# Kernel optimization log

Measured on AMD Instinct MI355X. Metric: run time of the kernel, lower is better.

## Reference

```python
import jax, jax.numpy as jnp
import numpy as np

NUM_DOCS = 1024  # fill_max of doc_indices

def setup_inputs() -> dict:
    key = jax.random.key(0)
    k1, k2, k3 = jax.random.split(key, 3)
    N, D, E = 262144, 1024, 64
    x = jax.random.normal(k1, (N, D), dtype=jnp.float32)
    doc_indices = jax.random.randint(k2, (N,), 0, NUM_DOCS, dtype=jnp.int64)
    W_gate = jax.random.normal(k3, (E, D), dtype=jnp.float32)
    return {"x": x, "doc_indices": doc_indices, "W_gate": W_gate}

def reference(x, doc_indices, W_gate):
    # gate linear + softmax: [N, E]
    logits = jnp.einsum('nd,ed->ne', x, W_gate)
    w = jax.nn.softmax(logits, axis=-1)

    seg = doc_indices.astype(jnp.int32)
    E = w.shape[-1]
    # one-pass segment reductions replacing the per-document Python loop
    sum_w = jax.ops.segment_sum(w, seg, num_segments=NUM_DOCS)          # [D, E]
    sum_w2 = jax.ops.segment_sum(w * w, seg, num_segments=NUM_DOCS)     # [D, E]
    counts = jax.ops.segment_sum(jnp.ones_like(w[:, :1]), seg, num_segments=NUM_DOCS)  # [D, 1]
    safe_n = jnp.maximum(counts, 1.0)
    centroid = sum_w / safe_n                                            # [D, E]
    # per-doc sum of squared deviations: sum(w^2) - n * centroid^2
    ssd = jnp.sum(sum_w2 - safe_n * centroid * centroid, axis=-1)        # [D]
    n = counts[:, 0]
    per_doc_mse = ssd / (safe_n[:, 0] * E)                               # mean over n_d*E elements
    valid = n > 1.0                                                      # docs with >1 token contribute
    penalty_sum = jnp.sum(jnp.where(valid, per_doc_mse, 0.0))
    num_unique = jnp.sum((n > 0.0).astype(jnp.float32))
    doc_penalty = penalty_sum / num_unique
    return (w, doc_penalty)
```

## Files before the change

### kernel.cpp

```cpp
#include <hip/hip_runtime.h>
#include <math.h>

#define NROWS 262144
#define DDIM  1024
#define EEXP  64
#define NDOCS 1024
#define BM    128
#define HB    64
#define RPB   (NROWS / HB)
#define NGEMM (NROWS / BM)

typedef __attribute__((ext_vector_type(8)))  __bf16 bf16x8;
typedef __attribute__((ext_vector_type(16))) float  f32x16;
typedef unsigned short ushort_t;
typedef unsigned int   uint_t;


__global__ __launch_bounds__(256) void conv_hist_kernel(const float* __restrict__ Wg,
                                                        ushort_t* __restrict__ Wf,
                                                        const int* __restrict__ idx,
                                                        int* __restrict__ hist_slices) {
    if (blockIdx.x < 512) {
        const int i = blockIdx.x * 256 + threadIdx.x;
        const int j = i & 7;
        const int l = (i >> 3) & 63;
        const int f = (i >> 9) & 7;
        const int T = i >> 12;
        const int cl = l & 31;
        const int hi = l >> 5;
        const int e  = cl + 32 * ((f >> 1) & 1);
        const int k  = T * 32 + 16 * (f & 1) + 8 * hi + j;
        const float wv = Wg[e * DDIM + k];
        const uint_t b = __float_as_uint(wv);
        ushort_t out;
        if (f < 4) {
            out = (ushort_t)(b >> 16);
        } else {
            const float lov = wv - __uint_as_float(b & 0xFFFF0000u);
            out = (ushort_t)(__float_as_uint(lov) >> 16);
        }
        Wf[i] = out;
    } else {
        __shared__ int lh[NDOCS];
        const int bh = blockIdx.x - 512;
        const int t  = threadIdx.x;
        for (int i = t; i < NDOCS; i += 256) lh[i] = 0;
        __syncthreads();
        const int base = bh * RPB;
        for (int i = t; i < RPB; i += 256) atomicAdd(&lh[idx[base + i]], 1);
        __syncthreads();
        for (int i = t; i < NDOCS; i += 256) hist_slices[bh * NDOCS + i] = lh[i];
    }
}

__global__ __launch_bounds__(1024) void scan_kernel(const int* __restrict__ hist_slices,
                                                    int* __restrict__ offsets,
                                                    int* __restrict__ cursor,
                                                    float* __restrict__ pen_sum,
                                                    float* __restrict__ uniq,
                                                    int* __restrict__ done_count) {
    __shared__ int sbuf[NDOCS];
    const int t = threadIdx.x;
    int my = 0;
    #pragma unroll 4
    for (int b = 0; b < HB; ++b) my += hist_slices[b * NDOCS + t];
    sbuf[t] = my;
    __syncthreads();
    for (int off = 1; off < NDOCS; off <<= 1) {
        int add = (t >= off) ? sbuf[t - off] : 0;
        __syncthreads();
        sbuf[t] += add;
        __syncthreads();
    }
    const int excl = sbuf[t] - my;
    offsets[t] = excl;
    cursor[t]  = excl;
    if (t == NDOCS - 1) offsets[NDOCS] = sbuf[t];
    if (t == 0) { pen_sum[0] = 0.0f; uniq[0] = 0.0f; done_count[0] = 0; }
}

__device__ __forceinline__ void gl2lds16(const float* g, float* l) {
    __builtin_amdgcn_global_load_lds(
        (const __attribute__((address_space(1))) void*)g,
        (__attribute__((address_space(3))) void*)l,
        16, 0, 0);
}

#define VMCNT(N)  asm volatile("s_waitcnt vmcnt(" #N ")" ::: "memory")

struct WT { bf16x8 h00, h01, h10, h11, m00, m01, m10, m11; };

__global__ __launch_bounds__(256, 2) void gemm_scatter_kernel(
    const float*    __restrict__ x,
    const ushort_t* __restrict__ Wf,
    const int*      __restrict__ idx,
    int*            __restrict__ cursor,
    int*            __restrict__ sorted_rows,
    float*          __restrict__ w_out)
{
    __shared__ float xs[2][8192];

    if (blockIdx.x >= NGEMM) {
        int* lh    = (int*)&xs[0][0];
        int* lbase = lh + NDOCS;
        int* lc    = lbase + NDOCS;
        const int bh = blockIdx.x - NGEMM;
        const int t  = threadIdx.x;
        for (int i = t; i < NDOCS; i += 256) { lh[i] = 0; lc[i] = 0; }
        __syncthreads();
        const int base = bh * RPB;
        for (int i = t; i < RPB; i += 256) atomicAdd(&lh[idx[base + i]], 1);
        __syncthreads();
        for (int i = t; i < NDOCS; i += 256) {
            const int c = lh[i];
            if (c) lbase[i] = atomicAdd(&cursor[i], c);
        }
        __syncthreads();
        for (int i = t; i < RPB; i += 256) {
            const int r = base + i;
            const int d = idx[r];
            const int p = atomicAdd(&lc[d], 1);
            sorted_rows[lbase[d] + p] = r;
        }
        return;
    }

    const int t   = threadIdx.x;
    const int w   = t >> 6;
    const int l   = t & 63;
    const int cl  = l & 31;
    const int hi  = l >> 5;
    const size_t br = (size_t)blockIdx.x * BM;

    f32x16 acc0 = {};
    f32x16 acc1 = {};
    WT wA, wB;

    union u8b { uint_t u[4]; bf16x8 v; };

#define LOAD_WF(DST, T2) do {                                                          \
        const ushort_t* p_ = Wf + ((size_t)(T2) * 8 * 64 + l) * 8;                     \
        DST.h00 = *(const bf16x8*)(p_ + 0 * 512);                                      \
        DST.h01 = *(const bf16x8*)(p_ + 1 * 512);                                      \
        DST.h10 = *(const bf16x8*)(p_ + 2 * 512);                                      \
        DST.h11 = *(const bf16x8*)(p_ + 3 * 512);                                      \
        DST.m00 = *(const bf16x8*)(p_ + 4 * 512);                                      \
        DST.m01 = *(const bf16x8*)(p_ + 5 * 512);                                      \
        DST.m10 = *(const bf16x8*)(p_ + 6 * 512);                                      \
        DST.m11 = *(const bf16x8*)(p_ + 7 * 512);                                      \
    } while (0)

#define STAGE_X2(BUF, SUP) do {                                                        \
        float* xb_ = &xs[BUF][w * 2048];                                               \
        _Pragma("unroll")                                                              \
        for (int i_ = 0; i_ < 8; ++i_) {                                               \
            const int row_ = i_ * 4 + (l >> 4);                                        \
            const int u_   = (l & 15) ^ (row_ & 15);                                   \
            const float* gp_ = x + (br + w * 32 + row_) * DDIM + (SUP) * 64 + u_ * 4;  \
            gl2lds16(gp_, xb_ + i_ * 256);                                             \
        } } while (0)

#define SPLIT8(A, B, AH, AL) do {                                                      \
        const float av_[8] = {A.x, A.y, A.z, A.w, B.x, B.y, B.z, B.w};                 \
        _Pragma("unroll")                                                              \
        for (int p_ = 0; p_ < 4; ++p_) {                                               \
            const uint_t b0_ = __float_as_uint(av_[2 * p_]);                           \
            const uint_t b1_ = __float_as_uint(av_[2 * p_ + 1]);                       \
            AH.u[p_] = (b0_ >> 16) | (b1_ & 0xFFFF0000u);                              \
            const float l0_ = av_[2 * p_]     - __uint_as_float(b0_ & 0xFFFF0000u);    \
            const float l1_ = av_[2 * p_ + 1] - __uint_as_float(b1_ & 0xFFFF0000u);    \
            AL.u[p_] = (__float_as_uint(l0_) >> 16) | (__float_as_uint(l1_) & 0xFFFF0000u); \
        } } while (0)

#define COMPUTE(BUF, TT, WV) do {                                                      \
        const float* xb_ = &xs[BUF][w * 2048];                                         \
        const int blk_ = (cl >> 2) * 256 + (cl & 3) * 64;                              \
        const int ku_  = (TT) * 8 + hi * 2;                                            \
        const int sw_  = cl & 15;                                                      \
        const float4 a0_ = *(const float4*)&xb_[blk_ + (((ku_ + 0) ^ sw_) * 4)];       \
        const float4 a1_ = *(const float4*)&xb_[blk_ + (((ku_ + 1) ^ sw_) * 4)];       \
        const float4 a2_ = *(const float4*)&xb_[blk_ + (((ku_ + 4) ^ sw_) * 4)];       \
        const float4 a3_ = *(const float4*)&xb_[blk_ + (((ku_ + 5) ^ sw_) * 4)];       \
        u8b ah0, al0, ah1, al1;                                                        \
        SPLIT8(a0_, a1_, ah0, al0);                                                    \
        SPLIT8(a2_, a3_, ah1, al1);                                                    \
        acc0 = __builtin_amdgcn_mfma_f32_32x32x16_bf16(ah0.v, WV.h00, acc0, 0, 0, 0);  \
        acc1 = __builtin_amdgcn_mfma_f32_32x32x16_bf16(ah0.v, WV.h10, acc1, 0, 0, 0);  \
        acc0 = __builtin_amdgcn_mfma_f32_32x32x16_bf16(ah0.v, WV.m00, acc0, 0, 0, 0);  \
        acc1 = __builtin_amdgcn_mfma_f32_32x32x16_bf16(ah0.v, WV.m10, acc1, 0, 0, 0);  \
        acc0 = __builtin_amdgcn_mfma_f32_32x32x16_bf16(al0.v, WV.h00, acc0, 0, 0, 0);  \
        acc1 = __builtin_amdgcn_mfma_f32_32x32x16_bf16(al0.v, WV.h10, acc1, 0, 0, 0);  \
        acc0 = __builtin_amdgcn_mfma_f32_32x32x16_bf16(ah1.v, WV.h01, acc0, 0, 0, 0);  \
        acc1 = __builtin_amdgcn_mfma_f32_32x32x16_bf16(ah1.v, WV.h11, acc1, 0, 0, 0);  \
        acc0 = __builtin_amdgcn_mfma_f32_32x32x16_bf16(ah1.v, WV.m01, acc0, 0, 0, 0);  \
        acc1 = __builtin_amdgcn_mfma_f32_32x32x16_bf16(ah1.v, WV.m11, acc1, 0, 0, 0);  \
        acc0 = __builtin_amdgcn_mfma_f32_32x32x16_bf16(al1.v, WV.h01, acc0, 0, 0, 0);  \
        acc1 = __builtin_amdgcn_mfma_f32_32x32x16_bf16(al1.v, WV.h11, acc1, 0, 0, 0);  \
    } while (0)

    LOAD_WF(wA, 0);
    STAGE_X2(0, 0);
    LOAD_WF(wB, 1);
    STAGE_X2(1, 1);
    VMCNT(16);
    COMPUTE(0, 0, wA);
    LOAD_WF(wA, 2);
    VMCNT(16);
    COMPUTE(0, 1, wB);

    #pragma unroll 1
    for (int S = 1; S < 15; ++S) {
        const int cb = S & 1;
        LOAD_WF(wB, 2 * S + 1);
        STAGE_X2(cb ^ 1, S + 1);
        VMCNT(16);
        COMPUTE(cb, 0, wA);
        LOAD_WF(wA, 2 * S + 2);
        VMCNT(16);
        COMPUTE(cb, 1, wB);
    }
    LOAD_WF(wB, 31);
    VMCNT(8);
    COMPUTE(1, 0, wA);
    VMCNT(0);
    COMPUTE(1, 1, wB);

    const size_t orow_base = br + (size_t)w * 32;
    #pragma unroll
    for (int r = 0; r < 16; ++r) {
        const int row = (r & 3) + 8 * (r >> 2) + 4 * hi;
        const float v0 = acc0[r];
        const float v1 = acc1[r];
        float m = fmaxf(v0, v1);
        m = fmaxf(m, __shfl_xor(m, 1));
        m = fmaxf(m, __shfl_xor(m, 2));
        m = fmaxf(m, __shfl_xor(m, 4));
        m = fmaxf(m, __shfl_xor(m, 8));
        m = fmaxf(m, __shfl_xor(m, 16));
        const float e0 = __expf(v0 - m);
        const float e1 = __expf(v1 - m);
        float s = e0 + e1;
        s += __shfl_xor(s, 1);
        s += __shfl_xor(s, 2);
        s += __shfl_xor(s, 4);
        s += __shfl_xor(s, 8);
        s += __shfl_xor(s, 16);
        const float inv = 1.0f / s;
        float* wo = w_out + (orow_base + row) * EEXP;
        wo[cl]      = e0 * inv;
        wo[32 + cl] = e1 * inv;
    }
#undef LOAD_WF
#undef STAGE_X2
#undef SPLIT8
#undef COMPUTE
}

__global__ __launch_bounds__(256) void segsum_final_kernel(
    const float* __restrict__ w,
    const int*   __restrict__ sorted_rows,
    const int*   __restrict__ offsets,
    float*       __restrict__ pen_sum,
    float*       __restrict__ uniq,
    int*         __restrict__ done_count,
    float*       __restrict__ pen_out)
{
    __shared__ int rows_s[512];
    __shared__ float ls1[4][64], ls2[4][64];

    const int d  = blockIdx.x;
    const int t  = threadIdx.x;
    const int e  = t & 63;
    const int rg = t >> 6;
    const int start = offsets[d];
    const int end   = offsets[d + 1];
    const int n     = end - start;

    for (int i = t; i < n && i < 512; i += 256) rows_s[i] = sorted_rows[start + i];
    __syncthreads();

    float s1 = 0.0f, s2 = 0.0f;
    for (int i = rg; i < n; i += 4) {
        const int row = (i < 512) ? rows_s[i] : sorted_rows[start + i];
        const float v = w[(size_t)row * EEXP + e];
        s1 += v;
        s2 += v * v;
    }

    ls1[rg][e] = s1;
    ls2[rg][e] = s2;
    __syncthreads();

    if (t < 64) {
        const float a = ls1[0][e] + ls1[1][e] + ls1[2][e] + ls1[3][e];
        const float b = ls2[0][e] + ls2[1][e] + ls2[2][e] + ls2[3][e];
        const float safe = fmaxf((float)n, 1.0f);
        float contrib = b - a * a / safe;
        #pragma unroll
        for (int off = 32; off > 0; off >>= 1)
            contrib += __shfl_down(contrib, off);
        if (e == 0) {
            if (n > 1) atomicAdd(pen_sum, contrib / (safe * (float)EEXP));
            if (n > 0) atomicAdd(uniq, 1.0f);
        }
    }
    __syncthreads();
    if (t == 0) {
        __threadfence();
        const int prev = atomicAdd(done_count, 1);
        if (prev == NDOCS - 1) {
            __threadfence();
            pen_out[0] = pen_sum[0] / uniq[0];
        }
    }
}

extern "C" void kernel_launch(void* const* d_in, const int* in_sizes, int n_in,
                              void* d_out, int out_size, void* d_ws, size_t ws_size,
                              hipStream_t stream) {
    const float* x   = (const float*)d_in[0];
    const int*   idx = (const int*)d_in[1];
    const float* Wg  = (const float*)d_in[2];

    float* out   = (float*)d_out;
    float* w_out = out;
    float* pen   = out + (size_t)NROWS * EEXP;

    ushort_t* Wf     = (ushort_t*)d_ws;
    int* hist_slices = (int*)(Wf + 131072);
    int* sorted_rows = hist_slices + HB * NDOCS;
    int* offsets     = sorted_rows + NROWS;
    int* cursor      = offsets + NDOCS + 1;
    float* pen_sum   = (float*)(cursor + NDOCS);
    float* uniq      = pen_sum + 1;
    int* done_count  = (int*)(uniq + 1);

    conv_hist_kernel<<<512 + HB, 256, 0, stream>>>(Wg, Wf, idx, hist_slices);
    scan_kernel<<<1, 1024, 0, stream>>>(hist_slices, offsets, cursor, pen_sum, uniq, done_count);
    gemm_scatter_kernel<<<NGEMM + HB, 256, 0, stream>>>(x, Wf, idx, cursor, sorted_rows, w_out);
    segsum_final_kernel<<<NDOCS, 256, 0, stream>>>(w_out, sorted_rows, offsets, pen_sum, uniq, done_count, pen);
}
```

Baseline: 360.5 us.

## Restructure gate GEMM into 16-row tiles with K-split across waves

Replaces the 128-row-per-block 32x32 MFMA GEMM with 16x16x32 MFMA tiles where each block covers 8 row-tiles of 16 rows. The four waves split the 64 experts and the K dimension is walked in 256-wide chunks with a per-block rotated start to spread Wf/x access. Softmax now goes through an LDS transpose buffer, and occupancy rises to 4 blocks per CU with a smaller LDS footprint. The histogram/scatter blocks move to the front of the grid. The intent is better latency hiding and more resident waves, at the cost of more barriers and reloading W for every 16-row tile.

```diff
diff --git a/kernel.cpp b/kernel.cpp
--- a/kernel.cpp
+++ b/kernel.cpp
@@ -5,13 +5,14 @@
 #define DDIM  1024
 #define EEXP  64
 #define NDOCS 1024
-#define BM    128
 #define HB    64
 #define RPB   (NROWS / HB)
-#define NGEMM (NROWS / BM)
-
-typedef __attribute__((ext_vector_type(8)))  __bf16 bf16x8;
-typedef __attribute__((ext_vector_type(16))) float  f32x16;
+#define BMT   16
+#define TPB   8
+#define NGEMM (NROWS / (BMT * TPB))
+
+typedef __attribute__((ext_vector_type(8))) __bf16 bf16x8;
+typedef __attribute__((ext_vector_type(4))) float  f32x4;
 typedef unsigned short ushort_t;
 typedef unsigned int   uint_t;
 
@@ -21,19 +22,18 @@
                                                         const int* __restrict__ idx,
                                                         int* __restrict__ hist_slices) {
     if (blockIdx.x < 512) {
-        const int i = blockIdx.x * 256 + threadIdx.x;
-        const int j = i & 7;
-        const int l = (i >> 3) & 63;
-        const int f = (i >> 9) & 7;
-        const int T = i >> 12;
-        const int cl = l & 31;
-        const int hi = l >> 5;
-        const int e  = cl + 32 * ((f >> 1) & 1);
-        const int k  = T * 32 + 16 * (f & 1) + 8 * hi + j;
+        const int i  = blockIdx.x * 256 + threadIdx.x;
+        const int j  = i & 7;
+        const int l  = (i >> 3) & 63;
+        const int hl = (i >> 9) & 1;
+        const int eb = (i >> 10) & 3;
+        const int Tg = i >> 12;
+        const int e  = eb * 16 + (l & 15);
+        const int k  = Tg * 32 + (l >> 4) * 8 + j;
         const float wv = Wg[e * DDIM + k];
         const uint_t b = __float_as_uint(wv);
         ushort_t out;
-        if (f < 4) {
+        if (hl == 0) {
             out = (ushort_t)(b >> 16);
         } else {
             const float lov = wv - __uint_as_float(b & 0xFFFF0000u);
@@ -87,10 +87,10 @@
 }
 
 #define VMCNT(N)  asm volatile("s_waitcnt vmcnt(" #N ")" ::: "memory")
-
-struct WT { bf16x8 h00, h01, h10, h11, m00, m01, m10, m11; };
-
-__global__ __launch_bounds__(256, 2) void gemm_scatter_kernel(
+#define LGKM0()   asm volatile("s_waitcnt lgkmcnt(0)" ::: "memory")
+#define BAR()     do { __builtin_amdgcn_s_barrier(); asm volatile("" ::: "memory"); } while (0)
+
+__global__ __launch_bounds__(256, 4) void gemm_scatter_kernel(
     const float*    __restrict__ x,
     const ushort_t* __restrict__ Wf,
     const int*      __restrict__ idx,
@@ -98,13 +98,14 @@
     int*            __restrict__ sorted_rows,
     float*          __restrict__ w_out)
 {
-    __shared__ float xs[2][8192];
-
-    if (blockIdx.x >= NGEMM) {
+    __shared__ float xs[2][BMT * 256];
+    __shared__ float lsm[BMT * 68];
+
+    if (blockIdx.x < HB) {
         int* lh    = (int*)&xs[0][0];
         int* lbase = lh + NDOCS;
         int* lc    = lbase + NDOCS;
-        const int bh = blockIdx.x - NGEMM;
+        const int bh = blockIdx.x;
         const int t  = threadIdx.x;
         for (int i = t; i < NDOCS; i += 256) { lh[i] = 0; lc[i] = 0; }
         __syncthreads();
@@ -125,39 +126,42 @@
         return;
     }
 
-    const int t   = threadIdx.x;
-    const int w   = t >> 6;
-    const int l   = t & 63;
-    const int cl  = l & 31;
-    const int hi  = l >> 5;
-    const size_t br = (size_t)blockIdx.x * BM;
-
-    f32x16 acc0 = {};
-    f32x16 acc1 = {};
-    WT wA, wB;
+    const int gb   = blockIdx.x - HB;
+    const int t    = threadIdx.x;
+    const int w    = t >> 6;
+    const int l    = t & 63;
+    const int al16 = l & 15;
+    const int g2   = l >> 4;
+    const size_t br = (size_t)gb * (BMT * TPB);
+    const int s0   = gb & 3;
+
+    f32x4 acc = {0.f, 0.f, 0.f, 0.f};
+    bf16x8 wh0, wl0, wh1, wl1, wh2, wl2, wh3, wl3, wh4, wl4, wh5, wl5, wh6, wl6, wh7, wl7;
 
     union u8b { uint_t u[4]; bf16x8 v; };
 
-#define LOAD_WF(DST, T2) do {                                                          \
-        const ushort_t* p_ = Wf + ((size_t)(T2) * 8 * 64 + l) * 8;                     \
-        DST.h00 = *(const bf16x8*)(p_ + 0 * 512);                                      \
-        DST.h01 = *(const bf16x8*)(p_ + 1 * 512);                                      \
-        DST.h10 = *(const bf16x8*)(p_ + 2 * 512);                                      \
-        DST.h11 = *(const bf16x8*)(p_ + 3 * 512);                                      \
-        DST.m00 = *(const bf16x8*)(p_ + 4 * 512);                                      \
-        DST.m01 = *(const bf16x8*)(p_ + 5 * 512);                                      \
-        DST.m10 = *(const bf16x8*)(p_ + 6 * 512);                                      \
-        DST.m11 = *(const bf16x8*)(p_ + 7 * 512);                                      \
+#define LWT(T2, WH, WL) do {                                                           \
+        const ushort_t* p_ = Wf + ((size_t)((T2) * 8 + w * 2) * 64 + l) * 8;           \
+        WH = *(const bf16x8*)p_;                                                       \
+        WL = *(const bf16x8*)(p_ + 512);                                               \
     } while (0)
 
-#define STAGE_X2(BUF, SUP) do {                                                        \
-        float* xb_ = &xs[BUF][w * 2048];                                               \
+#define LOAD_W_ALL(S) do {                                                             \
+        LWT((S)*8 + 0, wh0, wl0); LWT((S)*8 + 1, wh1, wl1);                            \
+        LWT((S)*8 + 2, wh2, wl2); LWT((S)*8 + 3, wh3, wl3);                            \
+        LWT((S)*8 + 4, wh4, wl4); LWT((S)*8 + 5, wh5, wl5);                            \
+        LWT((S)*8 + 6, wh6, wl6); LWT((S)*8 + 7, wh7, wl7);                            \
+    } while (0)
+
+#define STAGE(BUF, P) do {                                                             \
+        const int rb_ = ((P) >> 2) * BMT;                                              \
+        const int kb_ = ((s0 + ((P) & 3)) & 3) * 256;                                  \
+        float* xb_ = &xs[BUF][0];                                                      \
         _Pragma("unroll")                                                              \
-        for (int i_ = 0; i_ < 8; ++i_) {                                               \
-            const int row_ = i_ * 4 + (l >> 4);                                        \
-            const int u_   = (l & 15) ^ (row_ & 15);                                   \
-            const float* gp_ = x + (br + w * 32 + row_) * DDIM + (SUP) * 64 + u_ * 4;  \
-            gl2lds16(gp_, xb_ + i_ * 256);                                             \
+        for (int i_ = 0; i_ < 4; ++i_) {                                               \
+            const int rl_ = w * 4 + i_;                                                \
+            const float* gp_ = x + (br + rb_ + rl_) * (size_t)DDIM + kb_ + ((l ^ rl_) * 4); \
+            gl2lds16(gp_, xb_ + rl_ * 256);                                            \
         } } while (0)
 
 #define SPLIT8(A, B, AH, AL) do {                                                      \
@@ -172,88 +176,93 @@
             AL.u[p_] = (__float_as_uint(l0_) >> 16) | (__float_as_uint(l1_) & 0xFFFF0000u); \
         } } while (0)
 
-#define COMPUTE(BUF, TT, WV) do {                                                      \
-        const float* xb_ = &xs[BUF][w * 2048];                                         \
-        const int blk_ = (cl >> 2) * 256 + (cl & 3) * 64;                              \
-        const int ku_  = (TT) * 8 + hi * 2;                                            \
-        const int sw_  = cl & 15;                                                      \
-        const float4 a0_ = *(const float4*)&xb_[blk_ + (((ku_ + 0) ^ sw_) * 4)];       \
-        const float4 a1_ = *(const float4*)&xb_[blk_ + (((ku_ + 1) ^ sw_) * 4)];       \
-        const float4 a2_ = *(const float4*)&xb_[blk_ + (((ku_ + 4) ^ sw_) * 4)];       \
-        const float4 a3_ = *(const float4*)&xb_[blk_ + (((ku_ + 5) ^ sw_) * 4)];       \
-        u8b ah0, al0, ah1, al1;                                                        \
-        SPLIT8(a0_, a1_, ah0, al0);                                                    \
-        SPLIT8(a2_, a3_, ah1, al1);                                                    \
-        acc0 = __builtin_amdgcn_mfma_f32_32x32x16_bf16(ah0.v, WV.h00, acc0, 0, 0, 0);  \
-        acc1 = __builtin_amdgcn_mfma_f32_32x32x16_bf16(ah0.v, WV.h10, acc1, 0, 0, 0);  \
-        acc0 = __builtin_amdgcn_mfma_f32_32x32x16_bf16(ah0.v, WV.m00, acc0, 0, 0, 0);  \
-        acc1 = __builtin_amdgcn_mfma_f32_32x32x16_bf16(ah0.v, WV.m10, acc1, 0, 0, 0);  \
-        acc0 = __builtin_amdgcn_mfma_f32_32x32x16_bf16(al0.v, WV.h00, acc0, 0, 0, 0);  \
-        acc1 = __builtin_amdgcn_mfma_f32_32x32x16_bf16(al0.v, WV.h10, acc1, 0, 0, 0);  \
-        acc0 = __builtin_amdgcn_mfma_f32_32x32x16_bf16(ah1.v, WV.h01, acc0, 0, 0, 0);  \
-        acc1 = __builtin_amdgcn_mfma_f32_32x32x16_bf16(ah1.v, WV.h11, acc1, 0, 0, 0);  \
-        acc0 = __builtin_amdgcn_mfma_f32_32x32x16_bf16(ah1.v, WV.m01, acc0, 0, 0, 0);  \
-        acc1 = __builtin_amdgcn_mfma_f32_32x32x16_bf16(ah1.v, WV.m11, acc1, 0, 0, 0);  \
-        acc0 = __builtin_amdgcn_mfma_f32_32x32x16_bf16(al1.v, WV.h01, acc0, 0, 0, 0);  \
-        acc1 = __builtin_amdgcn_mfma_f32_32x32x16_bf16(al1.v, WV.h11, acc1, 0, 0, 0);  \
+#define KTILE(XB, TL, WH, WL) do {                                                     \
+        const int u0_ = ((TL) * 8 + g2 * 2)     ^ al16;                                \
+        const int u1_ = ((TL) * 8 + g2 * 2 + 1) ^ al16;                                \
+        const float4 a0_ = *(const float4*)&(XB)[al16 * 256 + u0_ * 4];                \
+        const float4 a1_ = *(const float4*)&(XB)[al16 * 256 + u1_ * 4];                \
+        u8b ah_, al_;                                                                  \
+        SPLIT8(a0_, a1_, ah_, al_);                                                    \
+        acc = __builtin_amdgcn_mfma_f32_16x16x32_bf16(ah_.v, WH, acc, 0, 0, 0);        \
+        acc = __builtin_amdgcn_mfma_f32_16x16x32_bf16(ah_.v, WL, acc, 0, 0, 0);        \
+        acc = __builtin_amdgcn_mfma_f32_16x16x32_bf16(al_.v, WH, acc, 0, 0, 0);        \
     } while (0)
 
-    LOAD_WF(wA, 0);
-    STAGE_X2(0, 0);
-    LOAD_WF(wB, 1);
-    STAGE_X2(1, 1);
-    VMCNT(16);
-    COMPUTE(0, 0, wA);
-    LOAD_WF(wA, 2);
-    VMCNT(16);
-    COMPUTE(0, 1, wB);
+#define EPILOGUE(TAU) do {                                                             \
+        _Pragma("unroll")                                                              \
+        for (int r_ = 0; r_ < 4; ++r_)                                                 \
+            lsm[(g2 * 4 + r_) * 68 + w * 16 + al16] = acc[r_];                         \
+        LGKM0(); BAR();                                                                \
+        const size_t rowg0_ = br + (size_t)(TAU) * BMT + w * 4;                        \
+        _Pragma("unroll")                                                              \
+        for (int rr_ = 0; rr_ < 4; ++rr_) {                                            \
+            const float v_ = lsm[(w * 4 + rr_) * 68 + l];                              \
+            float m_ = v_;                                                             \
+            m_ = fmaxf(m_, __shfl_xor(m_, 1));                                         \
+            m_ = fmaxf(m_, __shfl_xor(m_, 2));                                         \
+            m_ = fmaxf(m_, __shfl_xor(m_, 4));                                         \
+            m_ = fmaxf(m_, __shfl_xor(m_, 8));                                         \
+            m_ = fmaxf(m_, __shfl_xor(m_, 16));                                        \
+            m_ = fmaxf(m_, __shfl_xor(m_, 32));                                        \
+            const float e_ = __expf(v_ - m_);                                          \
+            float sden_ = e_;                                                          \
+            sden_ += __shfl_xor(sden_, 1);                                             \
+            sden_ += __shfl_xor(sden_, 2);                                             \
+            sden_ += __shfl_xor(sden_, 4);                                             \
+            sden_ += __shfl_xor(sden_, 8);                                             \
+            sden_ += __shfl_xor(sden_, 16);                                            \
+            sden_ += __shfl_xor(sden_, 32);                                            \
+            w_out[(rowg0_ + rr_) * EEXP + l] = e_ / sden_;                             \
+        }                                                                              \
+        acc = (f32x4){0.f, 0.f, 0.f, 0.f};                                             \
+    } while (0)
+
+    STAGE(0, 0);
 
     #pragma unroll 1
-    for (int S = 1; S < 15; ++S) {
-        const int cb = S & 1;
-        LOAD_WF(wB, 2 * S + 1);
-        STAGE_X2(cb ^ 1, S + 1);
+    for (int P = 0; P < 31; ++P) {
+        const int S = (s0 + (P & 3)) & 3;
+        const float* xb = &xs[P & 1][0];
+        LOAD_W_ALL(S);
         VMCNT(16);
-        COMPUTE(cb, 0, wA);
-        LOAD_WF(wA, 2 * S + 2);
+        BAR();
+        STAGE((P & 1) ^ 1, P + 1);
+        VMCNT(12);
+        KTILE(xb, 0, wh0, wl0);
+        KTILE(xb, 1, wh1, wl1);
+        KTILE(xb, 2, wh2, wl2);
+        KTILE(xb, 3, wh3, wl3);
+        VMCNT(4);
+        KTILE(xb, 4, wh4, wl4);
+        KTILE(xb, 5, wh5, wl5);
+        KTILE(xb, 6, wh6, wl6);
+        KTILE(xb, 7, wh7, wl7);
+        if ((P & 3) == 3) EPILOGUE(P >> 2);
+    }
+    {
+        const int S = (s0 + 3) & 3;
+        const float* xb = &xs[1][0];
+        LOAD_W_ALL(S);
         VMCNT(16);
-        COMPUTE(cb, 1, wB);
-    }
-    LOAD_WF(wB, 31);
-    VMCNT(8);
-    COMPUTE(1, 0, wA);
-    VMCNT(0);
-    COMPUTE(1, 1, wB);
-
-    const size_t orow_base = br + (size_t)w * 32;
-    #pragma unroll
-    for (int r = 0; r < 16; ++r) {
-        const int row = (r & 3) + 8 * (r >> 2) + 4 * hi;
-        const float v0 = acc0[r];
-        const float v1 = acc1[r];
-        float m = fmaxf(v0, v1);
-        m = fmaxf(m, __shfl_xor(m, 1));
-        m = fmaxf(m, __shfl_xor(m, 2));
-        m = fmaxf(m, __shfl_xor(m, 4));
-        m = fmaxf(m, __shfl_xor(m, 8));
-        m = fmaxf(m, __shfl_xor(m, 16));
-        const float e0 = __expf(v0 - m);
-        const float e1 = __expf(v1 - m);
-        float s = e0 + e1;
-        s += __shfl_xor(s, 1);
-        s += __shfl_xor(s, 2);
-        s += __shfl_xor(s, 4);
-        s += __shfl_xor(s, 8);
-        s += __shfl_xor(s, 16);
-        const float inv = 1.0f / s;
-        float* wo = w_out + (orow_base + row) * EEXP;
-        wo[cl]      = e0 * inv;
-        wo[32 + cl] = e1 * inv;
-    }
-#undef LOAD_WF
-#undef STAGE_X2
+        BAR();
+        VMCNT(8);
+        KTILE(xb, 0, wh0, wl0);
+        KTILE(xb, 1, wh1, wl1);
+        KTILE(xb, 2, wh2, wl2);
+        KTILE(xb, 3, wh3, wl3);
+        VMCNT(0);
+        KTILE(xb, 4, wh4, wl4);
+        KTILE(xb, 5, wh5, wl5);
+        KTILE(xb, 6, wh6, wl6);
+        KTILE(xb, 7, wh7, wl7);
+        EPILOGUE(7);
+    }
+#undef LWT
+#undef LOAD_W_ALL
+#undef STAGE
 #undef SPLIT8
-#undef COMPUTE
+#undef KTILE
+#undef EPILOGUE
 }
 
 __global__ __launch_bounds__(256) void segsum_final_kernel(
@@ -337,6 +346,6 @@
 
     conv_hist_kernel<<<512 + HB, 256, 0, stream>>>(Wg, Wf, idx, hist_slices);
     scan_kernel<<<1, 1024, 0, stream>>>(hist_slices, offsets, cursor, pen_sum, uniq, done_count);
-    gemm_scatter_kernel<<<NGEMM + HB, 256, 0, stream>>>(x, Wf, idx, cursor, sorted_rows, w_out);
+    gemm_scatter_kernel<<<HB + NGEMM, 256, 0, stream>>>(x, Wf, idx, cursor, sorted_rows, w_out);
     segsum_final_kernel<<<NDOCS, 256, 0, stream>>>(w_out, sorted_rows, offsets, pen_sum, uniq, done_count, pen);
 }
```

Result: slower. 484.7 us (+34.4%).
